# Performance work log

Measured on AMD Instinct MI355X. Metric: run time of the kernel, lower is better.

## Reference

```python
import jax, jax.numpy as jnp
import numpy as np

EMBED_DIM = 512
NUM_HEADS = 8
HEAD_DIM = EMBED_DIM // NUM_HEADS


def setup_inputs() -> dict:
    key = jax.random.key(0)
    ks = jax.random.split(key, 6)
    B, S, E = 2, 4096, EMBED_DIM
    scale = 1.0 / np.sqrt(E)
    return {
        "rotation_params": jax.random.normal(ks[0], (E, E), jnp.float32) * scale,
        "entangle_params": jax.random.normal(ks[1], (E, E), jnp.float32) * scale,
        "inputs": jax.random.normal(ks[2], (B, S, E), jnp.float32),
        "w_q": jax.random.normal(ks[3], (E, E), jnp.float32) * scale,
        "w_k": jax.random.normal(ks[4], (E, E), jnp.float32) * scale,
        "w_v": jax.random.normal(ks[5], (E, E), jnp.float32) * scale,
    }


def reference(rotation_params, entangle_params, inputs, w_q, w_k, w_v):
    B, S, E = inputs.shape
    H, D = NUM_HEADS, HEAD_DIM
    # torch nn.Linear(x) = x @ W.T ; then extra matmul with rotation/entangle mats
    q = (inputs @ w_q.T) @ rotation_params  # [B,S,E]
    k = (inputs @ w_k.T) @ entangle_params  # [B,S,E]
    v = inputs @ w_v.T                       # [B,S,E]
    # split heads -> [B,H,S,D]
    q = q.reshape(B, S, H, D).transpose(0, 2, 1, 3)
    k = k.reshape(B, S, H, D).transpose(0, 2, 1, 3)
    v = v.reshape(B, S, H, D).transpose(0, 2, 1, 3)
    scores = jnp.einsum("bhqd,bhkd->bhqk", q, k) / jnp.sqrt(jnp.float32(D))
    attn = jax.nn.softmax(scores, axis=-1)  # dropout p=0 (eval) -> identity
    out = jnp.einsum("bhqk,bhkd->bhqd", attn, v)
    return out.transpose(0, 2, 1, 3).reshape(B, S, E)
```

## Files before the change

### kernel.cpp

```cpp
#include <hip/hip_runtime.h>
#include <cstddef>

#define E 512
#define H 8
#define D 64
#define BATCH 2
#define SEQ 4096

typedef __attribute__((ext_vector_type(8))) short bf16x8;
typedef __attribute__((ext_vector_type(4))) float f32x4;
typedef __attribute__((ext_vector_type(16))) float f32x16;
typedef __attribute__((ext_vector_type(4))) unsigned uint4v;

__device__ __forceinline__ ushort f2bf(float f) {
  unsigned u = __builtin_bit_cast(unsigned, f);
  u += 0x7fff + ((u >> 16) & 1);
  return (ushort)(u >> 16);
}
__device__ __forceinline__ float bf2f(ushort h) {
  return __builtin_bit_cast(float, (unsigned)h << 16);
}
__device__ __forceinline__ unsigned pk_bf16(float lo, float hi) {
#if __has_builtin(__builtin_amdgcn_cvt_pk_bf16_f32)
  typedef __attribute__((ext_vector_type(2))) __bf16 bfv2;
  bfv2 r = __builtin_amdgcn_cvt_pk_bf16_f32(lo, hi);
  return __builtin_bit_cast(unsigned, r);
#else
  return (unsigned)f2bf(lo) | ((unsigned)f2bf(hi) << 16);
#endif
}
__device__ __forceinline__ float fexp2(float x) {
#if __has_builtin(__builtin_amdgcn_exp2f)
  return __builtin_amdgcn_exp2f(x);
#else
  return exp2f(x);
#endif
}
__device__ __forceinline__ void permswap32(unsigned& a, unsigned& b) {
  asm("v_permlane32_swap_b32 %0, %1" : "+v"(a), "+v"(b));
}

__global__ __launch_bounds__(256) void xcast(const float* __restrict__ x,
                                             ushort* __restrict__ xh,
                                             ushort* __restrict__ xl) {
  size_t i = ((size_t)blockIdx.x * 256 + threadIdx.x) * 4;
  float4 v = *(const float4*)&x[i];
  ushort4 h, l;
  h.x = f2bf(v.x); l.x = f2bf(v.x - bf2f(h.x));
  h.y = f2bf(v.y); l.y = f2bf(v.y - bf2f(h.y));
  h.z = f2bf(v.z); l.z = f2bf(v.z - bf2f(h.z));
  h.w = f2bf(v.w); l.w = f2bf(v.w - bf2f(h.w));
  *(ushort4*)&xh[i] = h;
  *(ushort4*)&xl[i] = l;
}

__global__ __launch_bounds__(256) void fold_tiled(
    const float* __restrict__ wq, const float* __restrict__ wk,
    const float* __restrict__ rot, const float* __restrict__ ent,
    ushort* __restrict__ weffbT) {
  const int which = blockIdx.z;
  const float* w = which ? wk : wq;
  const float* r = which ? ent : rot;
  const int k = blockIdx.x * 256 + threadIdx.x;
  const int n0 = blockIdx.y * 8;
  float acc[8] = {};
  for (int j0 = 0; j0 < E; j0 += 16) {
    float wv_[16];
#pragma unroll
    for (int u = 0; u < 16; ++u) wv_[u] = w[(size_t)(j0 + u) * E + k];
#pragma unroll
    for (int u = 0; u < 16; ++u)
#pragma unroll
      for (int t = 0; t < 8; ++t)
        acc[t] += wv_[u] * r[(size_t)(j0 + u) * E + n0 + t];
  }
#pragma unroll
  for (int t = 0; t < 8; ++t)
    weffbT[(size_t)which * E * E + (size_t)(n0 + t) * E + k] = f2bf(acc[t]);
}

__global__ __launch_bounds__(256) void wv_cast(const float* __restrict__ wv,
                                               ushort* __restrict__ dst) {
  size_t i = ((size_t)blockIdx.x * 256 + threadIdx.x) * 4;
  float4 v = *(const float4*)&wv[i];
  ushort4 o;
  o.x = f2bf(v.x); o.y = f2bf(v.y); o.z = f2bf(v.z); o.w = f2bf(v.w);
  *(ushort4*)&dst[i] = o;
}

#define LDA 40

__global__ __launch_bounds__(256) void qkv_fused(
    const ushort* __restrict__ xhg, const ushort* __restrict__ xlg,
    const ushort* __restrict__ weffbT, ushort* __restrict__ qg,
    ushort* __restrict__ kg, ushort* __restrict__ vtg) {
  __shared__ ushort sm[5 * 64 * LDA];
  ushort* Ah = sm;
  ushort* Al = sm + 64 * LDA;
  ushort* Bs = sm + 2 * 64 * LDA;
  ushort* vt_tile = Bs;

  const int head = blockIdx.x;
  const int m0 = blockIdx.y * 64;
  const int tid = threadIdx.x;
  const int wave = tid >> 6, lane = tid & 63;
  const int l15 = lane & 15, quad = lane >> 4;
  const int ar = tid >> 2, ac8 = (tid & 3) * 8;

  const ushort* arow = xhg + (size_t)(m0 + ar) * E + ac8;
  const ushort* lrow = xlg + (size_t)(m0 + ar) * E + ac8;
  const ushort* b0row = weffbT + (size_t)(head * 64 + ar) * E + ac8;

  f32x4 acc[3][4];
#pragma unroll
  for (int w = 0; w < 3; ++w)
#pragma unroll
    for (int nt = 0; nt < 4; ++nt) acc[w][nt] = (f32x4){0.f, 0.f, 0.f, 0.f};

  uint4 pa_h = *(const uint4*)&arow[0];
  uint4 pa_l = *(const uint4*)&lrow[0];
  uint4 pb0 = *(const uint4*)&b0row[0];
  uint4 pb1 = *(const uint4*)&b0row[E * E];
  uint4 pb2 = *(const uint4*)&b0row[2 * E * E];

  for (int k0 = 0; k0 < E; k0 += 32) {
    __syncthreads();
    *(uint4*)&Ah[ar * LDA + ac8] = pa_h;
    *(uint4*)&Al[ar * LDA + ac8] = pa_l;
    *(uint4*)&Bs[0 * 64 * LDA + ar * LDA + ac8] = pb0;
    *(uint4*)&Bs[1 * 64 * LDA + ar * LDA + ac8] = pb1;
    *(uint4*)&Bs[2 * 64 * LDA + ar * LDA + ac8] = pb2;
    __syncthreads();

    const int kn = (k0 + 32 < E) ? k0 + 32 : 0;
    pa_h = *(const uint4*)&arow[kn];
    pa_l = *(const uint4*)&lrow[kn];
    pb0 = *(const uint4*)&b0row[kn];
    pb1 = *(const uint4*)&b0row[E * E + kn];
    pb2 = *(const uint4*)&b0row[2 * E * E + kn];

    bf16x8 ah = *(const bf16x8*)&Ah[(wave * 16 + l15) * LDA + quad * 8];
    bf16x8 al = *(const bf16x8*)&Al[(wave * 16 + l15) * LDA + quad * 8];
#pragma unroll
    for (int w = 0; w < 3; ++w)
#pragma unroll
      for (int nt = 0; nt < 4; ++nt) {
        bf16x8 bf = *(const bf16x8*)&Bs[w * 64 * LDA + (nt * 16 + l15) * LDA +
                                        quad * 8];
        acc[w][nt] =
            __builtin_amdgcn_mfma_f32_16x16x32_bf16(ah, bf, acc[w][nt], 0, 0, 0);
        acc[w][nt] =
            __builtin_amdgcn_mfma_f32_16x16x32_bf16(al, bf, acc[w][nt], 0, 0, 0);
      }
  }

  const int b = m0 >> 12;
  const int s_base = m0 & (SEQ - 1);
  const float QSCALE = 0.125f * 1.44269504f;

#pragma unroll
  for (int w = 0; w < 2; ++w) {
    ushort* dst = (w == 0) ? qg : kg;
    float sc = (w == 0) ? QSCALE : 1.0f;
#pragma unroll
    for (int nt = 0; nt < 4; ++nt)
#pragma unroll
      for (int r = 0; r < 4; ++r) {
        float v = acc[w][nt][r] * sc;
        float vo = __shfl_xor(v, 1);
        if (!(lane & 1)) {
          int s = s_base + wave * 16 + quad * 4 + r;
          size_t ix = ((size_t)(b * H + head) * SEQ + s) * D + nt * 16 + l15;
          *(unsigned*)&dst[ix] = pk_bf16(v, vo);
        }
      }
  }

  __syncthreads();
#pragma unroll
  for (int nt = 0; nt < 4; ++nt) {
    uint2 w2;
    w2.x = pk_bf16(acc[2][nt][0], acc[2][nt][1]);
    w2.y = pk_bf16(acc[2][nt][2], acc[2][nt][3]);
    *(uint2*)&vt_tile[(nt * 16 + l15) * 72 + wave * 16 + quad * 4] = w2;
  }
  __syncthreads();
  {
    int vr = tid >> 2, vs = (tid & 3) * 16;
    uint4 c0 = *(const uint4*)&vt_tile[vr * 72 + vs];
    uint4 c1 = *(const uint4*)&vt_tile[vr * 72 + vs + 8];
    size_t vo = ((size_t)(b * H + head) * D + vr) * SEQ + s_base + vs;
    *(uint4*)&vtg[vo] = c0;
    *(uint4*)&vtg[vo + 8] = c1;
  }
}

#define LDK 72

__global__ __launch_bounds__(512, 4) void attn_mfma(
    const ushort* __restrict__ qg, const ushort* __restrict__ kg,
    const ushort* __restrict__ vtg, float* __restrict__ out) {
  __shared__ ushort sm[4 * 64 * LDK + 256];
  ushort* Ks0 = sm;
  ushort* Vs0 = sm + 2 * 64 * LDK;
  float* lex = (float*)(sm + 4 * 64 * LDK);

  const int qt = blockIdx.x;
  const int bh = blockIdx.y;
  const int tid = threadIdx.x;
  const int wave = tid >> 6;
  const int grp = wave >> 2, wq = wave & 3;
  const int lane = tid & 63;
  const int l31 = lane & 31, hi = lane >> 5;
  const int gtid = tid & 255;

  const ushort* qp = qg + (size_t)bh * SEQ * D;
  const ushort* kp = kg + (size_t)bh * SEQ * D;
  const ushort* vp = vtg + (size_t)bh * D * SEQ;
  ushort* Ksg = Ks0 + grp * 64 * LDK;
  ushort* Vsg = Vs0 + grp * 64 * LDK;

  const int qrow0 = qt * 128 + wq * 32;
  bf16x8 qf[4];
#pragma unroll
  for (int ds = 0; ds < 4; ++ds)
    qf[ds] =
        *(const bf16x8*)&qp[(size_t)(qrow0 + l31) * D + ds * 16 + hi * 8];

  f32x16 o[2];
  o[0] = 0.f;
  o[1] = 0.f;
  float l_r = 0.f;

  const int r0 = gtid >> 3, c0 = (gtid & 7) * 8;
  const int r1 = 32 + r0;

  uint4 pk0 = *(const uint4*)&kp[(size_t)(grp * 64 + r0) * D + c0];
  uint4 pk1 = *(const uint4*)&kp[(size_t)(grp * 64 + r1) * D + c0];
  uint4 pv0 = *(const uint4*)&vp[(size_t)r0 * SEQ + grp * 64 + c0];
  uint4 pv1 = *(const uint4*)&vp[(size_t)r1 * SEQ + grp * 64 + c0];

  for (int it = 0; it < SEQ / 128; ++it) {
    __syncthreads();
    *(uint4*)&Ksg[r0 * LDK + c0] = pk0;
    *(uint4*)&Ksg[r1 * LDK + c0] = pk1;
    *(uint4*)&Vsg[r0 * LDK + c0] = pv0;
    *(uint4*)&Vsg[r1 * LDK + c0] = pv1;
    __syncthreads();

    {
      const int itn = (it + 1 < SEQ / 128) ? it + 1 : it;
      const int ktn = itn * 2 + grp;
      const ushort* ksrc = kp + (size_t)ktn * 64 * D;
      pk0 = *(const uint4*)&ksrc[r0 * D + c0];
      pk1 = *(const uint4*)&ksrc[r1 * D + c0];
      pv0 = *(const uint4*)&vp[(size_t)r0 * SEQ + ktn * 64 + c0];
      pv1 = *(const uint4*)&vp[(size_t)r1 * SEQ + ktn * 64 + c0];
    }

    __builtin_amdgcn_s_setprio(1);
    f32x16 st0 = 0.f, st1 = 0.f;
#pragma unroll
    for (int ds = 0; ds < 4; ++ds) {
      bf16x8 kf0 = *(const bf16x8*)&Ksg[(l31)*LDK + ds * 16 + hi * 8];
      bf16x8 kf1 = *(const bf16x8*)&Ksg[(32 + l31) * LDK + ds * 16 + hi * 8];
      st0 = __builtin_amdgcn_mfma_f32_32x32x16_bf16(kf0, qf[ds], st0, 0, 0, 0);
      st1 = __builtin_amdgcn_mfma_f32_32x32x16_bf16(kf1, qf[ds], st1, 0, 0, 0);
    }

    bf16x8 pf00, pf01;
    {
      float pv[16];
#pragma unroll
      for (int r = 0; r < 16; ++r) pv[r] = fexp2(st0[r]);
      float s01 = (pv[0] + pv[1]) + (pv[2] + pv[3]);
      float s23 = (pv[4] + pv[5]) + (pv[6] + pv[7]);
      float s45 = (pv[8] + pv[9]) + (pv[10] + pv[11]);
      float s67 = (pv[12] + pv[13]) + (pv[14] + pv[15]);
      l_r += (s01 + s23) + (s45 + s67);
      unsigned w0[4], w1[4];
#pragma unroll
      for (int j = 0; j < 2; ++j) {
        {
          unsigned c0w = pk_bf16(pv[2 * j + 0], pv[2 * j + 1]);
          unsigned c1w = pk_bf16(pv[2 * j + 4], pv[2 * j + 5]);
          permswap32(c0w, c1w);
          w0[j] = c0w;
          w0[2 + j] = c1w;
        }
        {
          unsigned c0w = pk_bf16(pv[2 * j + 8], pv[2 * j + 9]);
          unsigned c1w = pk_bf16(pv[2 * j + 12], pv[2 * j + 13]);
          permswap32(c0w, c1w);
          w1[j] = c0w;
          w1[2 + j] = c1w;
        }
      }
      pf00 = __builtin_bit_cast(bf16x8, (uint4v){w0[0], w0[1], w0[2], w0[3]});
      pf01 = __builtin_bit_cast(bf16x8, (uint4v){w1[0], w1[1], w1[2], w1[3]});
    }
#pragma unroll
    for (int nt = 0; nt < 2; ++nt) {
      bf16x8 vf0 = *(const bf16x8*)&Vsg[(nt * 32 + l31) * LDK + hi * 8];
      o[nt] =
          __builtin_amdgcn_mfma_f32_32x32x16_bf16(pf00, vf0, o[nt], 0, 0, 0);
      bf16x8 vf1 = *(const bf16x8*)&Vsg[(nt * 32 + l31) * LDK + 16 + hi * 8];
      o[nt] =
          __builtin_amdgcn_mfma_f32_32x32x16_bf16(pf01, vf1, o[nt], 0, 0, 0);
    }

    bf16x8 pf10, pf11;
    {
      float pv[16];
#pragma unroll
      for (int r = 0; r < 16; ++r) pv[r] = fexp2(st1[r]);
      float s01 = (pv[0] + pv[1]) + (pv[2] + pv[3]);
      float s23 = (pv[4] + pv[5]) + (pv[6] + pv[7]);
      float s45 = (pv[8] + pv[9]) + (pv[10] + pv[11]);
      float s67 = (pv[12] + pv[13]) + (pv[14] + pv[15]);
      l_r += (s01 + s23) + (s45 + s67);
      unsigned w0[4], w1[4];
#pragma unroll
      for (int j = 0; j < 2; ++j) {
        {
          unsigned c0w = pk_bf16(pv[2 * j + 0], pv[2 * j + 1]);
          unsigned c1w = pk_bf16(pv[2 * j + 4], pv[2 * j + 5]);
          permswap32(c0w, c1w);
          w0[j] = c0w;
          w0[2 + j] = c1w;
        }
        {
          unsigned c0w = pk_bf16(pv[2 * j + 8], pv[2 * j + 9]);
          unsigned c1w = pk_bf16(pv[2 * j + 12], pv[2 * j + 13]);
          permswap32(c0w, c1w);
          w1[j] = c0w;
          w1[2 + j] = c1w;
        }
      }
      pf10 = __builtin_bit_cast(bf16x8, (uint4v){w0[0], w0[1], w0[2], w0[3]});
      pf11 = __builtin_bit_cast(bf16x8, (uint4v){w1[0], w1[1], w1[2], w1[3]});
    }
#pragma unroll
    for (int nt = 0; nt < 2; ++nt) {
      bf16x8 vf0 = *(const bf16x8*)&Vsg[(nt * 32 + l31) * LDK + 32 + hi * 8];
      o[nt] =
          __builtin_amdgcn_mfma_f32_32x32x16_bf16(pf10, vf0, o[nt], 0, 0, 0);
      bf16x8 vf1 = *(const bf16x8*)&Vsg[(nt * 32 + l31) * LDK + 48 + hi * 8];
      o[nt] =
          __builtin_amdgcn_mfma_f32_32x32x16_bf16(pf11, vf1, o[nt], 0, 0, 0);
    }
    __builtin_amdgcn_s_setprio(0);
  }

  __syncthreads();
  float lg = l_r + __shfl_xor(l_r, 32);
  float* Oex = (float*)sm;
  if (grp == 1) {
#pragma unroll
    for (int nt = 0; nt < 2; ++nt)
#pragma unroll
      for (int r = 0; r < 16; ++r) {
        int row = (r & 3) + 8 * (r >> 2) + 4 * hi;
        Oex[(wq * 32 + row) * 68 + nt * 32 + l31] = o[nt][r];
      }
    if (lane < 32) lex[wq * 32 + l31] = lg;
  }
  __syncthreads();
  if (grp == 0) {
    float linv = 1.f / (lg + lex[wq * 32 + l31]);
    const int b = bh >> 3, h = bh & 7;
#pragma unroll
    for (int r = 0; r < 16; ++r) {
      int row = (r & 3) + 8 * (r >> 2) + 4 * hi;
      float inv = __shfl(linv, row);
      int srow = qt * 128 + wq * 32 + row;
#pragma unroll
      for (int nt = 0; nt < 2; ++nt) {
        float val = o[nt][r] + Oex[(wq * 32 + row) * 68 + nt * 32 + l31];
        out[((size_t)b * SEQ + srow) * E + h * D + nt * 32 + l31] = val * inv;
      }
    }
  }
}

extern "C" void kernel_launch(void* const* d_in, const int* in_sizes, int n_in,
                              void* d_out, int out_size, void* d_ws,
                              size_t ws_size, hipStream_t stream) {
  const float* rot = (const float*)d_in[0];
  const float* ent = (const float*)d_in[1];
  const float* x = (const float*)d_in[2];
  const float* wq = (const float*)d_in[3];
  const float* wk = (const float*)d_in[4];
  const float* wv = (const float*)d_in[5];
  float* out = (float*)d_out;

  const size_t NX = (size_t)BATCH * SEQ * E;
  ushort* weffbT = (ushort*)d_ws;
  ushort* xh = weffbT + 3 * E * E;
  ushort* xl = xh + NX;
  ushort* qg = xl + NX;
  ushort* kg = qg + NX;
  ushort* vtg = kg + NX;

  xcast<<<dim3(NX / 1024), 256, 0, stream>>>(x, xh, xl);
  fold_tiled<<<dim3(E / 256, E / 8, 2), 256, 0, stream>>>(wq, wk, rot, ent,
                                                          weffbT);
  wv_cast<<<dim3(E * E / 1024), 256, 0, stream>>>(wv, weffbT + 2 * E * E);
  qkv_fused<<<dim3(H, BATCH * SEQ / 64), 256, 0, stream>>>(xh, xl, weffbT, qg,
                                                           kg, vtg);
  attn_mfma<<<dim3(SEQ / 128, BATCH * H), 512, 0, stream>>>(qg, kg, vtg, out);
}
```

Baseline: 263.0 us.

## Retile QKV projection to 128-row blocks with 32x32 MFMA and 8 waves

The QKV projection kernel now processes 128 rows per block with 512 threads. Waves are arranged 4x2 over a 128x192 output tile and issue 32x32x16 bf16 MFMAs instead of 16x16x32. The aim is more reuse per LDS load and fewer redundant loads of the weight tiles, since grid blocks are halved. The V-transpose epilogue is adapted to the new layout. The cost is more LDS and register pressure per block, and half as many blocks.

```diff
diff --git a/kernel.cpp b/kernel.cpp
--- a/kernel.cpp
+++ b/kernel.cpp
@@ -88,70 +88,78 @@
   *(ushort4*)&dst[i] = o;
 }
 
-#define LDA 40
-
-__global__ __launch_bounds__(256) void qkv_fused(
+#define LDQ 72
+#define LDS_S 136
+
+__global__ __launch_bounds__(512, 4) void qkv_fused(
     const ushort* __restrict__ xhg, const ushort* __restrict__ xlg,
     const ushort* __restrict__ weffbT, ushort* __restrict__ qg,
     ushort* __restrict__ kg, ushort* __restrict__ vtg) {
-  __shared__ ushort sm[5 * 64 * LDA];
+  __shared__ ushort sm[(128 + 128 + 192) * LDQ];
   ushort* Ah = sm;
-  ushort* Al = sm + 64 * LDA;
-  ushort* Bs = sm + 2 * 64 * LDA;
-  ushort* vt_tile = Bs;
+  ushort* Al = sm + 128 * LDQ;
+  ushort* Bs = sm + 256 * LDQ;
+  ushort* vt_lds = Bs;
 
   const int head = blockIdx.x;
-  const int m0 = blockIdx.y * 64;
+  const int m0 = blockIdx.y * 128;
   const int tid = threadIdx.x;
   const int wave = tid >> 6, lane = tid & 63;
-  const int l15 = lane & 15, quad = lane >> 4;
+  const int l31 = lane & 31, hi = lane >> 5;
+  const int wm = wave & 3, wn = wave >> 2;
+
   const int ar = tid >> 2, ac8 = (tid & 3) * 8;
+  const int b1r = tid >> 2;
+  const int b2r = 128 + ((tid >> 2) & 63);
 
   const ushort* arow = xhg + (size_t)(m0 + ar) * E + ac8;
   const ushort* lrow = xlg + (size_t)(m0 + ar) * E + ac8;
-  const ushort* b0row = weffbT + (size_t)(head * 64 + ar) * E + ac8;
-
-  f32x4 acc[3][4];
-#pragma unroll
-  for (int w = 0; w < 3; ++w)
-#pragma unroll
-    for (int nt = 0; nt < 4; ++nt) acc[w][nt] = (f32x4){0.f, 0.f, 0.f, 0.f};
+  const ushort* b1row =
+      weffbT + (size_t)(b1r >> 6) * E * E + (size_t)(head * 64 + (b1r & 63)) * E + ac8;
+  const ushort* b2row =
+      weffbT + (size_t)2 * E * E + (size_t)(head * 64 + (b2r & 63)) * E + ac8;
+
+  f32x16 acc[3];
+  acc[0] = 0.f;
+  acc[1] = 0.f;
+  acc[2] = 0.f;
 
   uint4 pa_h = *(const uint4*)&arow[0];
   uint4 pa_l = *(const uint4*)&lrow[0];
-  uint4 pb0 = *(const uint4*)&b0row[0];
-  uint4 pb1 = *(const uint4*)&b0row[E * E];
-  uint4 pb2 = *(const uint4*)&b0row[2 * E * E];
+  uint4 pb1 = *(const uint4*)&b1row[0];
+  uint4 pb2 = *(const uint4*)&b2row[0];
+
+  const ushort* Ar = Ah + (wm * 32 + l31) * LDQ;
+  const ushort* Lr = Al + (wm * 32 + l31) * LDQ;
+  const ushort* Br = Bs + (wn * 96 + l31) * LDQ;
 
   for (int k0 = 0; k0 < E; k0 += 32) {
     __syncthreads();
-    *(uint4*)&Ah[ar * LDA + ac8] = pa_h;
-    *(uint4*)&Al[ar * LDA + ac8] = pa_l;
-    *(uint4*)&Bs[0 * 64 * LDA + ar * LDA + ac8] = pb0;
-    *(uint4*)&Bs[1 * 64 * LDA + ar * LDA + ac8] = pb1;
-    *(uint4*)&Bs[2 * 64 * LDA + ar * LDA + ac8] = pb2;
+    *(uint4*)&Ah[ar * LDQ + ac8] = pa_h;
+    *(uint4*)&Al[ar * LDQ + ac8] = pa_l;
+    *(uint4*)&Bs[b1r * LDQ + ac8] = pb1;
+    if (tid < 256) *(uint4*)&Bs[b2r * LDQ + ac8] = pb2;
     __syncthreads();
 
     const int kn = (k0 + 32 < E) ? k0 + 32 : 0;
     pa_h = *(const uint4*)&arow[kn];
     pa_l = *(const uint4*)&lrow[kn];
-    pb0 = *(const uint4*)&b0row[kn];
-    pb1 = *(const uint4*)&b0row[E * E + kn];
-    pb2 = *(const uint4*)&b0row[2 * E * E + kn];
-
-    bf16x8 ah = *(const bf16x8*)&Ah[(wave * 16 + l15) * LDA + quad * 8];
-    bf16x8 al = *(const bf16x8*)&Al[(wave * 16 + l15) * LDA + quad * 8];
-#pragma unroll
-    for (int w = 0; w < 3; ++w)
-#pragma unroll
-      for (int nt = 0; nt < 4; ++nt) {
-        bf16x8 bf = *(const bf16x8*)&Bs[w * 64 * LDA + (nt * 16 + l15) * LDA +
-                                        quad * 8];
-        acc[w][nt] =
-            __builtin_amdgcn_mfma_f32_16x16x32_bf16(ah, bf, acc[w][nt], 0, 0, 0);
-        acc[w][nt] =
-            __builtin_amdgcn_mfma_f32_16x16x32_bf16(al, bf, acc[w][nt], 0, 0, 0);
-      }
+    pb1 = *(const uint4*)&b1row[kn];
+    pb2 = *(const uint4*)&b2row[kn];
+
+#pragma unroll
+    for (int ks = 0; ks < 2; ++ks) {
+      bf16x8 ah = *(const bf16x8*)&Ar[ks * 16 + hi * 8];
+      bf16x8 al = *(const bf16x8*)&Lr[ks * 16 + hi * 8];
+#pragma unroll
+      for (int t = 0; t < 3; ++t) {
+        bf16x8 bf = *(const bf16x8*)&Br[t * 32 * LDQ + ks * 16 + hi * 8];
+        acc[t] =
+            __builtin_amdgcn_mfma_f32_32x32x16_bf16(ah, bf, acc[t], 0, 0, 0);
+        acc[t] =
+            __builtin_amdgcn_mfma_f32_32x32x16_bf16(al, bf, acc[t], 0, 0, 0);
+      }
+    }
   }
 
   const int b = m0 >> 12;
@@ -159,36 +167,46 @@
   const float QSCALE = 0.125f * 1.44269504f;
 
 #pragma unroll
-  for (int w = 0; w < 2; ++w) {
-    ushort* dst = (w == 0) ? qg : kg;
-    float sc = (w == 0) ? QSCALE : 1.0f;
-#pragma unroll
-    for (int nt = 0; nt < 4; ++nt)
-#pragma unroll
-      for (int r = 0; r < 4; ++r) {
-        float v = acc[w][nt][r] * sc;
+  for (int t = 0; t < 3; ++t) {
+    const int n0 = wn * 96 + t * 32;
+    const int w = n0 >> 6;
+    if (w != 2) {
+      ushort* dst = (w == 0) ? qg : kg;
+      const float sc = (w == 0) ? QSCALE : 1.0f;
+      const int d = (n0 & 63) + l31;
+#pragma unroll
+      for (int r = 0; r < 16; ++r) {
+        float v = acc[t][r] * sc;
         float vo = __shfl_xor(v, 1);
         if (!(lane & 1)) {
-          int s = s_base + wave * 16 + quad * 4 + r;
-          size_t ix = ((size_t)(b * H + head) * SEQ + s) * D + nt * 16 + l15;
+          int s = s_base + wm * 32 + (r & 3) + 8 * (r >> 2) + 4 * hi;
+          size_t ix = ((size_t)(b * H + head) * SEQ + s) * D + d;
           *(unsigned*)&dst[ix] = pk_bf16(v, vo);
         }
       }
+    }
   }
 
   __syncthreads();
-#pragma unroll
-  for (int nt = 0; nt < 4; ++nt) {
-    uint2 w2;
-    w2.x = pk_bf16(acc[2][nt][0], acc[2][nt][1]);
-    w2.y = pk_bf16(acc[2][nt][2], acc[2][nt][3]);
-    *(uint2*)&vt_tile[(nt * 16 + l15) * 72 + wave * 16 + quad * 4] = w2;
+  if (wn == 1) {
+#pragma unroll
+    for (int t = 1; t < 3; ++t) {
+      const int d = (t - 1) * 32 + l31;
+#pragma unroll
+      for (int g = 0; g < 4; ++g) {
+        uint2 w2;
+        w2.x = pk_bf16(acc[t][g * 4 + 0], acc[t][g * 4 + 1]);
+        w2.y = pk_bf16(acc[t][g * 4 + 2], acc[t][g * 4 + 3]);
+        int s = wm * 32 + 8 * g + 4 * hi;
+        *(uint2*)&vt_lds[d * LDS_S + s] = w2;
+      }
+    }
   }
   __syncthreads();
   {
-    int vr = tid >> 2, vs = (tid & 3) * 16;
-    uint4 c0 = *(const uint4*)&vt_tile[vr * 72 + vs];
-    uint4 c1 = *(const uint4*)&vt_tile[vr * 72 + vs + 8];
+    int vr = tid >> 3, vs = (tid & 7) * 16;
+    uint4 c0 = *(const uint4*)&vt_lds[vr * LDS_S + vs];
+    uint4 c1 = *(const uint4*)&vt_lds[vr * LDS_S + vs + 8];
     size_t vo = ((size_t)(b * H + head) * D + vr) * SEQ + s_base + vs;
     *(uint4*)&vtg[vo] = c0;
     *(uint4*)&vtg[vo + 8] = c1;
@@ -406,7 +424,7 @@
   fold_tiled<<<dim3(E / 256, E / 8, 2), 256, 0, stream>>>(wq, wk, rot, ent,
                                                           weffbT);
   wv_cast<<<dim3(E * E / 1024), 256, 0, stream>>>(wv, weffbT + 2 * E * E);
-  qkv_fused<<<dim3(H, BATCH * SEQ / 64), 256, 0, stream>>>(xh, xl, weffbT, qg,
-                                                           kg, vtg);
+  qkv_fused<<<dim3(H, BATCH * SEQ / 128), 512, 0, stream>>>(xh, xl, weffbT, qg,
+                                                            kg, vtg);
   attn_mfma<<<dim3(SEQ / 128, BATCH * H), 512, 0, stream>>>(qg, kg, vtg, out);
 }
```

New measurement: 241.4 us. -8.2%, faster.
